# Performance work log

Hardware: AMD Instinct MI355X
Metric: run time of the kernel (lower is better)

## Reference

```python
import jax, jax.numpy as jnp
import numpy as np

N, E, D, K = 50000, 800000, 128, 128


def _graph_conv(x, src, dst, w, W_rel, b_rel, W_root, n_nodes):
    # PyG GraphConv (aggr='add'): out = lin_rel(sum_j w_ij * x_j) + lin_root(x)
    msg = w[:, None] * x[src]                              # [E, D]
    agg = jax.ops.segment_sum(msg, dst, num_segments=n_nodes)  # [N, D]
    return agg @ W_rel + b_rel + x @ W_root


def setup_inputs() -> dict:
    key = jax.random.key(0)
    ks = jax.random.split(key, 16)
    sc = 1.0 / np.sqrt(D).astype(np.float32)
    inp = {
        "x": jax.random.normal(ks[0], (N, D), dtype=jnp.float32),
        "edge_index": jax.random.randint(ks[1], (2, E), 0, N, dtype=jnp.int64 if jax.config.jax_enable_x64 else jnp.int32),
        "edge_weight": jax.random.uniform(ks[2], (E,), dtype=jnp.float32),
        # GraphConv layer 1
        "W_rel1": jax.random.normal(ks[3], (D, D), dtype=jnp.float32) * sc,
        "b_rel1": jnp.zeros((D,), dtype=jnp.float32),
        "W_root1": jax.random.normal(ks[4], (D, D), dtype=jnp.float32) * sc,
        # GraphConv layer 2
        "W_rel2": jax.random.normal(ks[5], (D, D), dtype=jnp.float32) * sc,
        "b_rel2": jnp.zeros((D,), dtype=jnp.float32),
        "W_root2": jax.random.normal(ks[6], (D, D), dtype=jnp.float32) * sc,
        # MLP: Linear(D,128) + Identity, then final Linear(128,K)
        "W_m1": jax.random.normal(ks[7], (D, 128), dtype=jnp.float32) * sc,
        "b_m1": jnp.zeros((128,), dtype=jnp.float32),
        "W_out": jax.random.normal(ks[8], (128, K), dtype=jnp.float32) * (1.0 / np.sqrt(128).astype(np.float32)),
        "b_out": jnp.zeros((K,), dtype=jnp.float32),
    }
    return inp


def reference(x, edge_index, edge_weight, W_rel1, b_rel1, W_root1,
              W_rel2, b_rel2, W_root2, W_m1, b_m1, W_out, b_out):
    n_nodes = x.shape[0]
    src, dst = edge_index[0], edge_index[1]

    # Message passing stack with ReLU
    h = jax.nn.relu(_graph_conv(x, src, dst, edge_weight, W_rel1, b_rel1, W_root1, n_nodes))
    h = jax.nn.relu(_graph_conv(h, src, dst, edge_weight, W_rel2, b_rel2, W_root2, n_nodes))

    # MLP -> cluster logits (mlp_act = Identity)
    s = (h @ W_m1 + b_m1) @ W_out + b_out                  # [N, K]
    probs = jax.nn.softmax(s, axis=-1)                     # [N, K]

    # dense_mincut_pool losses (computed edge-wise; A = to_dense_adj(edge_index, w))
    # degree d_i = sum_j A[i, j] = scatter of w over src
    deg = jax.ops.segment_sum(edge_weight, src, num_segments=n_nodes)  # [N]
    # mincut_num = trace(S^T A S) = sum_e w_e * <S[src_e], S[dst_e]>
    mincut_num = jnp.einsum('e,ek,ek->', edge_weight, probs[src], probs[dst])
    # mincut_den = trace(S^T D S) = sum_i d_i * ||S_i||^2
    mincut_den = jnp.sum(deg * jnp.sum(probs * probs, axis=-1))
    mc_loss = -(mincut_num / mincut_den)

    # orthogonality loss: || SS/||SS||_F - I/sqrt(K) ||_F
    ss = probs.T @ probs                                   # [K, K]
    k = probs.shape[1]
    o_loss = jnp.linalg.norm(ss / jnp.linalg.norm(ss) - jnp.eye(k, dtype=ss.dtype) / np.float32(np.sqrt(k)))

    return probs, mc_loss, o_loss
```

## Files before the change

### kernel.cpp

```cpp
#include <hip/hip_runtime.h>
#include <hip/hip_bf16.h>

#define D 128
#define KT 32
#define SS_BLOCKS 256
#define NUM_BLOCKS 2048

__device__ __forceinline__ float bfl(unsigned u) { return __uint_as_float(u << 16); }
__device__ __forceinline__ float bfh(unsigned u) { return __uint_as_float(u & 0xffff0000u); }
__device__ __forceinline__ unsigned short f2b(float f) {
    unsigned u = __float_as_uint(f);
    return (unsigned short)((u + 0x7fffu + ((u >> 16) & 1u)) >> 16);
}

__global__ __launch_bounds__(256) void f2bf_kernel(const float* __restrict__ in,
                                                   unsigned short* __restrict__ out, int n8) {
    int i = blockIdx.x * 256 + threadIdx.x;
    if (i < n8) {
        float4 a = ((const float4*)in)[2 * i];
        float4 b = ((const float4*)in)[2 * i + 1];
        ushort4 lo = make_ushort4(f2b(a.x), f2b(a.y), f2b(a.z), f2b(a.w));
        ushort4 hi = make_ushort4(f2b(b.x), f2b(b.y), f2b(b.z), f2b(b.w));
        ((ushort4*)out)[2 * i] = lo;
        ((ushort4*)out)[2 * i + 1] = hi;
    }
}

__global__ __launch_bounds__(256) void hist_deg_kernel(const int* __restrict__ src,
                                                       const int* __restrict__ dst,
                                                       const float* __restrict__ w,
                                                       int* __restrict__ cnt,
                                                       float* __restrict__ deg,
                                                       int* __restrict__ slot, int E) {
    int e = blockIdx.x * 256 + threadIdx.x;
    if (e < E) {
        slot[e] = atomicAdd(&cnt[dst[e]], 1);
        atomicAdd(&deg[src[e]], w[e]);
    }
}

__global__ __launch_bounds__(256) void scan_chunk_kernel(const int* __restrict__ cnt,
                                                         int* __restrict__ rowptr,
                                                         int* __restrict__ aux, int N) {
    __shared__ int ts[256];
    int t = threadIdx.x;
    int base = blockIdx.x * 1024 + t * 4;
    int v[4], s = 0;
#pragma unroll
    for (int i = 0; i < 4; ++i) {
        v[i] = (base + i < N) ? cnt[base + i] : 0;
        s += v[i];
    }
    ts[t] = s;
    __syncthreads();
#pragma unroll
    for (int off = 1; off < 256; off <<= 1) {
        int add = (t >= off) ? ts[t - off] : 0;
        __syncthreads();
        ts[t] += add;
        __syncthreads();
    }
    int run = ts[t] - s;
#pragma unroll
    for (int i = 0; i < 4; ++i) {
        run += v[i];
        if (base + i < N) rowptr[base + i + 1] = run;
    }
    if (t == 255) aux[blockIdx.x] = ts[255];
}

__global__ void scan_aux_kernel(int* __restrict__ aux, int nb) {
    if (threadIdx.x == 0) {
        int s = 0;
        for (int i = 0; i < nb; ++i) { s += aux[i]; aux[i] = s; }
    }
}

__global__ __launch_bounds__(256) void add_off_kernel(int* __restrict__ rowptr,
                                                      const int* __restrict__ aux, int N) {
    int i = blockIdx.x * 256 + threadIdx.x;
    if (i == 0) rowptr[0] = 0;
    if (i < N) {
        int b = i >> 10;
        if (b > 0) rowptr[i + 1] += aux[b - 1];
    }
}

__global__ __launch_bounds__(256) void fill_kernel(const int* __restrict__ src,
                                                   const int* __restrict__ dst,
                                                   const float* __restrict__ w,
                                                   const int* __restrict__ rowptr,
                                                   const int* __restrict__ slot,
                                                   int* __restrict__ csr_src,
                                                   float* __restrict__ csr_w, int E) {
    int e = blockIdx.x * 256 + threadIdx.x;
    if (e < E) {
        int pos = rowptr[dst[e]] + slot[e];
        csr_src[pos] = src[e];
        csr_w[pos] = w[e];
    }
}

__global__ __launch_bounds__(256) void gatherq_kernel(const unsigned short* __restrict__ xh,
                                                      const int* __restrict__ csr_src,
                                                      const float* __restrict__ csr_w,
                                                      const int* __restrict__ rowptr,
                                                      float* __restrict__ agg, int N) {
    int node = blockIdx.x * 4 + (threadIdx.x >> 6);
    if (node >= N) return;
    int lane = threadIdx.x & 63;
    int q = lane >> 4;
    int c8 = (lane & 15) * 8;
    int beg = rowptr[node], end = rowptr[node + 1];
    float a[4][8];
#pragma unroll
    for (int i = 0; i < 4; ++i)
#pragma unroll
        for (int k = 0; k < 8; ++k) a[i][k] = 0.f;
    int j = beg;
    for (; j + 15 < end; j += 16) {
        int si[4]; float wi[4]; uint4 qv[4];
#pragma unroll
        for (int i = 0; i < 4; ++i) {
            int e = j + 4 * i + q;
            si[i] = csr_src[e];
            wi[i] = csr_w[e];
        }
#pragma unroll
        for (int i = 0; i < 4; ++i) qv[i] = *(const uint4*)&xh[(size_t)si[i] * D + c8];
#pragma unroll
        for (int i = 0; i < 4; ++i) {
            a[i][0] += wi[i] * bfl(qv[i].x); a[i][1] += wi[i] * bfh(qv[i].x);
            a[i][2] += wi[i] * bfl(qv[i].y); a[i][3] += wi[i] * bfh(qv[i].y);
            a[i][4] += wi[i] * bfl(qv[i].z); a[i][5] += wi[i] * bfh(qv[i].z);
            a[i][6] += wi[i] * bfl(qv[i].w); a[i][7] += wi[i] * bfh(qv[i].w);
        }
    }
    for (; j + 3 < end; j += 4) {
        int e = j + q;
        int s0 = csr_src[e]; float w0 = csr_w[e];
        uint4 qv = *(const uint4*)&xh[(size_t)s0 * D + c8];
        a[0][0] += w0 * bfl(qv.x); a[0][1] += w0 * bfh(qv.x);
        a[0][2] += w0 * bfl(qv.y); a[0][3] += w0 * bfh(qv.y);
        a[0][4] += w0 * bfl(qv.z); a[0][5] += w0 * bfh(qv.z);
        a[0][6] += w0 * bfl(qv.w); a[0][7] += w0 * bfh(qv.w);
    }
    int rem = end - j;
    if (q < rem) {
        int e = j + q;
        int s0 = csr_src[e]; float w0 = csr_w[e];
        uint4 qv = *(const uint4*)&xh[(size_t)s0 * D + c8];
        a[1][0] += w0 * bfl(qv.x); a[1][1] += w0 * bfh(qv.x);
        a[1][2] += w0 * bfl(qv.y); a[1][3] += w0 * bfh(qv.y);
        a[1][4] += w0 * bfl(qv.z); a[1][5] += w0 * bfh(qv.z);
        a[1][6] += w0 * bfl(qv.w); a[1][7] += w0 * bfh(qv.w);
    }
    float r[8];
#pragma unroll
    for (int k = 0; k < 8; ++k) {
        r[k] = a[0][k] + a[1][k] + a[2][k] + a[3][k];
        r[k] += __shfl_xor(r[k], 16);
        r[k] += __shfl_xor(r[k], 32);
    }
    if (lane < 16) {
        *(float4*)&agg[(size_t)node * D + c8]     = make_float4(r[0], r[1], r[2], r[3]);
        *(float4*)&agg[(size_t)node * D + c8 + 4] = make_float4(r[4], r[5], r[6], r[7]);
    }
}

#define FMA4(acc, a, wv) { acc.x += (a) * (wv).x; acc.y += (a) * (wv).y; \
                           acc.z += (a) * (wv).z; acc.w += (a) * (wv).w; }

__global__ __launch_bounds__(256) void lin_kernel(const float* __restrict__ A1,
                                                  const float* __restrict__ A2,
                                                  const float* __restrict__ W1,
                                                  const float* __restrict__ W2,
                                                  const float* __restrict__ b,
                                                  float* __restrict__ out,
                                                  unsigned short* __restrict__ outh, int N) {
    __shared__ float As[KT][132];
    __shared__ float Ws[KT][D];
    int tid = threadIdx.x;
    int r0 = blockIdx.x * 128;
    int ty4 = (tid >> 3) * 4;
    int tx16 = (tid & 7) * 16;

    float4 acc[4][4];
#pragma unroll
    for (int i = 0; i < 4; ++i)
#pragma unroll
        for (int j = 0; j < 4; ++j) acc[i][j] = make_float4(0.f, 0.f, 0.f, 0.f);

    for (int t = 0; t < 8; ++t) {
        const float* A = (t < 4) ? A1 : A2;
        const float* W = (t < 4) ? W1 : W2;
        int koff = (t & 3) * KT;
        __syncthreads();
#pragma unroll
        for (int i = 0; i < 4; ++i) {
            int f4 = tid + i * 256;
            int row = f4 >> 3;
            int c4 = f4 & 7;
            float4 v = make_float4(0.f, 0.f, 0.f, 0.f);
            if (r0 + row < N) v = *(const float4*)&A[(size_t)(r0 + row) * D + koff + c4 * 4];
            As[c4 * 4 + 0][row] = v.x;
            As[c4 * 4 + 1][row] = v.y;
            As[c4 * 4 + 2][row] = v.z;
            As[c4 * 4 + 3][row] = v.w;
        }
#pragma unroll
        for (int i = 0; i < 4; ++i) {
            int f4 = tid + i * 256;
            int k = f4 >> 5;
            int c4 = f4 & 31;
            *(float4*)&Ws[k][c4 * 4] = *(const float4*)&W[(size_t)(koff + k) * D + c4 * 4];
        }
        __syncthreads();
#pragma unroll 4
        for (int k = 0; k < KT; ++k) {
            float4 av = *(const float4*)&As[k][ty4];
            float4 w0 = *(const float4*)&Ws[k][tx16];
            float4 w1 = *(const float4*)&Ws[k][tx16 + 4];
            float4 w2 = *(const float4*)&Ws[k][tx16 + 8];
            float4 w3 = *(const float4*)&Ws[k][tx16 + 12];
            FMA4(acc[0][0], av.x, w0); FMA4(acc[0][1], av.x, w1);
            FMA4(acc[0][2], av.x, w2); FMA4(acc[0][3], av.x, w3);
            FMA4(acc[1][0], av.y, w0); FMA4(acc[1][1], av.y, w1);
            FMA4(acc[1][2], av.y, w2); FMA4(acc[1][3], av.y, w3);
            FMA4(acc[2][0], av.z, w0); FMA4(acc[2][1], av.z, w1);
            FMA4(acc[2][2], av.z, w2); FMA4(acc[2][3], av.z, w3);
            FMA4(acc[3][0], av.w, w0); FMA4(acc[3][1], av.w, w1);
            FMA4(acc[3][2], av.w, w2); FMA4(acc[3][3], av.w, w3);
        }
    }
    float4 bv[4];
#pragma unroll
    for (int j = 0; j < 4; ++j) bv[j] = *(const float4*)&b[tx16 + j * 4];
#pragma unroll
    for (int i = 0; i < 4; ++i) {
        int r = r0 + ty4 + i;
        if (r < N) {
#pragma unroll
            for (int j = 0; j < 4; ++j) {
                float4 v;
                v.x = fmaxf(acc[i][j].x + bv[j].x, 0.f);
                v.y = fmaxf(acc[i][j].y + bv[j].y, 0.f);
                v.z = fmaxf(acc[i][j].z + bv[j].z, 0.f);
                v.w = fmaxf(acc[i][j].w + bv[j].w, 0.f);
                *(float4*)&out[(size_t)r * D + tx16 + j * 4] = v;
                if (outh) {
                    ushort4 u = make_ushort4(f2b(v.x), f2b(v.y), f2b(v.z), f2b(v.w));
                    *(ushort4*)&outh[(size_t)r * D + tx16 + j * 4] = u;
                }
            }
        }
    }
}

__global__ __launch_bounds__(256) void smallmm_kernel(const float* __restrict__ Wm1,
                                                      const float* __restrict__ bm1,
                                                      const float* __restrict__ Wout,
                                                      const float* __restrict__ bout,
                                                      float* __restrict__ Wc,
                                                      float* __restrict__ bc) {
    int idx = blockIdx.x * 256 + threadIdx.x;
    if (blockIdx.x < 64) {
        int i = idx >> 7, j = idx & 127;
        float s = 0.f;
        for (int k = 0; k < 128; ++k) s += Wm1[i * 128 + k] * Wout[k * 128 + j];
        Wc[idx] = s;
    } else {
        int j = threadIdx.x;
        if (j < 128) {
            float s = bout[j];
            for (int k = 0; k < 128; ++k) s += bm1[k] * Wout[k * 128 + j];
            bc[j] = s;
        }
    }
}

__global__ __launch_bounds__(256) void out_softmax_kernel(const float* __restrict__ h2,
                                                          const float* __restrict__ Wc,
                                                          const float* __restrict__ bc,
                                                          const float* __restrict__ deg,
                                                          float* __restrict__ probs,
                                                          unsigned short* __restrict__ pbh,
                                                          float* __restrict__ accum, int N) {
    __shared__ float Rs[32][128];
    __shared__ float Ws[128 * 64];
    int tid = threadIdx.x;
    int wave = tid >> 6, lane = tid & 63;
    int r0 = blockIdx.x * 32;
#pragma unroll
    for (int i = 0; i < 4; ++i) {
        int f4 = tid + i * 256;
        int row = f4 >> 5;
        int c4 = f4 & 31;
        float4 v = make_float4(0.f, 0.f, 0.f, 0.f);
        if (r0 + row < N) v = *(const float4*)&h2[(size_t)(r0 + row) * D + c4 * 4];
        *(float4*)&Rs[row][c4 * 4] = v;
    }
    float lg[8][2];
#pragma unroll
    for (int h = 0; h < 2; ++h) {
        __syncthreads();
#pragma unroll
        for (int i = 0; i < 8; ++i) {
            int f4 = tid + i * 256;
            int k = f4 >> 4;
            int c4 = f4 & 15;
            *(float4*)&Ws[k * 64 + c4 * 4] = *(const float4*)&Wc[(size_t)k * 128 + h * 64 + c4 * 4];
        }
        __syncthreads();
        float bv = bc[h * 64 + lane];
        float a[8];
#pragma unroll
        for (int ri = 0; ri < 8; ++ri) a[ri] = bv;
        for (int k = 0; k < 128; ++k) {
            float wv = Ws[k * 64 + lane];
#pragma unroll
            for (int ri = 0; ri < 8; ++ri) a[ri] += Rs[wave + ri * 4][k] * wv;
        }
#pragma unroll
        for (int ri = 0; ri < 8; ++ri) lg[ri][h] = a[ri];
    }
    float den_local = 0.f;
#pragma unroll
    for (int ri = 0; ri < 8; ++ri) {
        int row = wave + ri * 4;
        int gr = r0 + row;
        float m = fmaxf(lg[ri][0], lg[ri][1]);
#pragma unroll
        for (int s = 32; s >= 1; s >>= 1) m = fmaxf(m, __shfl_xor(m, s));
        float e0 = expf(lg[ri][0] - m);
        float e1 = expf(lg[ri][1] - m);
        float sum = e0 + e1;
#pragma unroll
        for (int s = 32; s >= 1; s >>= 1) sum += __shfl_xor(sum, s);
        float inv = 1.f / sum;
        float p0 = e0 * inv, p1 = e1 * inv;
        float sq = p0 * p0 + p1 * p1;
#pragma unroll
        for (int s = 32; s >= 1; s >>= 1) sq += __shfl_xor(sq, s);
        if (gr < N) {
            probs[(size_t)gr * D + lane]      = p0;
            probs[(size_t)gr * D + 64 + lane] = p1;
            pbh[(size_t)gr * D + lane]      = f2b(p0);
            pbh[(size_t)gr * D + 64 + lane] = f2b(p1);
            if (lane == 0) den_local += deg[gr] * sq;
        }
    }
    if (lane == 0 && den_local != 0.f) atomicAdd(&accum[1], den_local);
}

__global__ __launch_bounds__(256) void num_ss_kernel(const float* __restrict__ probs,
                                                     const unsigned short* __restrict__ pbh,
                                                     const int* __restrict__ csr_src,
                                                     const float* __restrict__ csr_w,
                                                     const int* __restrict__ rowptr,
                                                     float* __restrict__ accum,
                                                     float* __restrict__ partial, int N) {
    int tid = threadIdx.x;
    if (blockIdx.x < SS_BLOCKS) {
        __shared__ float Ps[32][132];
        int a0 = (tid >> 4) * 8;
        int b0 = (tid & 15) * 8;
        float acc[8][8];
#pragma unroll
        for (int i = 0; i < 8; ++i)
#pragma unroll
            for (int j = 0; j < 8; ++j) acc[i][j] = 0.f;

        int rowsPerBlk = (N + SS_BLOCKS - 1) / SS_BLOCKS;
        int rbeg = blockIdx.x * rowsPerBlk;
        int rend = rbeg + rowsPerBlk;
        if (rend > N) rend = N;

        for (int c = rbeg; c < rend; c += 32) {
            int nr = rend - c;
            if (nr > 32) nr = 32;
            __syncthreads();
            for (int i = tid; i < nr * 32; i += 256) {
                int r = i >> 5, c4 = i & 31;
                *(float4*)&Ps[r][c4 * 4] = *(const float4*)&probs[(size_t)(c + r) * D + c4 * 4];
            }
            __syncthreads();
            for (int r = 0; r < nr; ++r) {
                float4 av0 = *(const float4*)&Ps[r][a0];
                float4 av1 = *(const float4*)&Ps[r][a0 + 4];
                float4 bv0 = *(const float4*)&Ps[r][b0];
                float4 bv1 = *(const float4*)&Ps[r][b0 + 4];
                float av[8] = {av0.x, av0.y, av0.z, av0.w, av1.x, av1.y, av1.z, av1.w};
                float bv[8] = {bv0.x, bv0.y, bv0.z, bv0.w, bv1.x, bv1.y, bv1.z, bv1.w};
#pragma unroll
                for (int i = 0; i < 8; ++i)
#pragma unroll
                    for (int j = 0; j < 8; ++j) acc[i][j] += av[i] * bv[j];
            }
        }
        float* pb = partial + (size_t)blockIdx.x * 16384;
#pragma unroll
        for (int i = 0; i < 8; ++i) {
            *(float4*)&pb[(a0 + i) * 128 + b0]     = make_float4(acc[i][0], acc[i][1], acc[i][2], acc[i][3]);
            *(float4*)&pb[(a0 + i) * 128 + b0 + 4] = make_float4(acc[i][4], acc[i][5], acc[i][6], acc[i][7]);
        }
        return;
    }
    int bid = blockIdx.x - SS_BLOCKS;
    int wave = tid >> 6, lane = tid & 63;
    int q = lane >> 4;
    int c8 = (lane & 15) * 8;
    float acc = 0.f;
    int stride = NUM_BLOCKS * 4;
    for (int node = bid * 4 + wave; node < N; node += stride) {
        float4 pdA = *(const float4*)&probs[(size_t)node * D + c8];
        float4 pdB = *(const float4*)&probs[(size_t)node * D + c8 + 4];
        int beg = rowptr[node], end = rowptr[node + 1];
        int j = beg;
        for (; j + 15 < end; j += 16) {
            int si[4]; float wi[4]; uint4 qv[4];
#pragma unroll
            for (int i = 0; i < 4; ++i) {
                int e = j + 4 * i + q;
                si[i] = csr_src[e];
                wi[i] = csr_w[e];
            }
#pragma unroll
            for (int i = 0; i < 4; ++i) qv[i] = *(const uint4*)&pbh[(size_t)si[i] * D + c8];
#pragma unroll
            for (int i = 0; i < 4; ++i) {
                acc += wi[i] * (bfl(qv[i].x) * pdA.x + bfh(qv[i].x) * pdA.y
                              + bfl(qv[i].y) * pdA.z + bfh(qv[i].y) * pdA.w
                              + bfl(qv[i].z) * pdB.x + bfh(qv[i].z) * pdB.y
                              + bfl(qv[i].w) * pdB.z + bfh(qv[i].w) * pdB.w);
            }
        }
        for (; j + 3 < end; j += 4) {
            int e = j + q;
            int s0 = csr_src[e]; float w0 = csr_w[e];
            uint4 qv = *(const uint4*)&pbh[(size_t)s0 * D + c8];
            acc += w0 * (bfl(qv.x) * pdA.x + bfh(qv.x) * pdA.y
                       + bfl(qv.y) * pdA.z + bfh(qv.y) * pdA.w
                       + bfl(qv.z) * pdB.x + bfh(qv.z) * pdB.y
                       + bfl(qv.w) * pdB.z + bfh(qv.w) * pdB.w);
        }
        int rem = end - j;
        if (q < rem) {
            int e = j + q;
            int s0 = csr_src[e]; float w0 = csr_w[e];
            uint4 qv = *(const uint4*)&pbh[(size_t)s0 * D + c8];
            acc += w0 * (bfl(qv.x) * pdA.x + bfh(qv.x) * pdA.y
                       + bfl(qv.y) * pdA.z + bfh(qv.y) * pdA.w
                       + bfl(qv.z) * pdB.x + bfh(qv.z) * pdB.y
                       + bfl(qv.w) * pdB.z + bfh(qv.w) * pdB.w);
        }
    }
#pragma unroll
    for (int m = 32; m >= 1; m >>= 1) acc += __shfl_xor(acc, m);
    if (lane == 0 && acc != 0.f) atomicAdd(&accum[0], acc);
}

__global__ __launch_bounds__(256) void ss_reduce_kernel(const float* __restrict__ partial,
                                                        float* __restrict__ ss) {
    int i = blockIdx.x * 256 + threadIdx.x;
    float s = 0.f;
    for (int b = 0; b < SS_BLOCKS; ++b) s += partial[(size_t)b * 16384 + i];
    ss[i] = s;
}

__global__ __launch_bounds__(256) void finalize_kernel(const float* __restrict__ ss,
                                                       const float* __restrict__ accum,
                                                       float* __restrict__ out2) {
    int tid = threadIdx.x;
    __shared__ float wsum[4], wsum2[4];
    float s = 0.f;
    for (int i = tid; i < 16384; i += 256) { float v = ss[i]; s += v * v; }
#pragma unroll
    for (int m = 32; m >= 1; m >>= 1) s += __shfl_xor(s, m);
    if ((tid & 63) == 0) wsum[tid >> 6] = s;
    __syncthreads();
    float norm = sqrtf(wsum[0] + wsum[1] + wsum[2] + wsum[3]);
    float inv = 1.f / norm;
    const float rk = 0.08838834764831845f;
    float o = 0.f;
    for (int i = tid; i < 16384; i += 256) {
        int a = i >> 7, b = i & 127;
        float v = ss[i] * inv - (a == b ? rk : 0.f);
        o += v * v;
    }
#pragma unroll
    for (int m = 32; m >= 1; m >>= 1) o += __shfl_xor(o, m);
    if ((tid & 63) == 0) wsum2[tid >> 6] = o;
    __syncthreads();
    if (tid == 0) {
        out2[0] = -(accum[0] / accum[1]);
        out2[1] = sqrtf(wsum2[0] + wsum2[1] + wsum2[2] + wsum2[3]);
    }
}

extern "C" void kernel_launch(void* const* d_in, const int* in_sizes, int n_in,
                              void* d_out, int out_size, void* d_ws, size_t ws_size,
                              hipStream_t stream) {
    const float* x      = (const float*)d_in[0];
    const int*   ei     = (const int*)d_in[1];
    const float* w      = (const float*)d_in[2];
    const float* Wrel1  = (const float*)d_in[3];
    const float* brel1  = (const float*)d_in[4];
    const float* Wroot1 = (const float*)d_in[5];
    const float* Wrel2  = (const float*)d_in[6];
    const float* brel2  = (const float*)d_in[7];
    const float* Wroot2 = (const float*)d_in[8];
    const float* Wm1    = (const float*)d_in[9];
    const float* bm1    = (const float*)d_in[10];
    const float* Wout   = (const float*)d_in[11];
    const float* bout   = (const float*)d_in[12];

    int N = in_sizes[0] / D;
    int E = in_sizes[2];
    const int* src = ei;
    const int* dst = ei + E;

    float* probs = (float*)d_out;
    float* out2  = probs + (size_t)N * D;
    float* h2    = probs;

    float* ws    = (float*)d_ws;
    float* agg   = ws;
    float* h1    = ws + (size_t)N * D;
    float* Wc    = ws + (size_t)2 * N * D;
    float* bc    = Wc + 16384;
    float* ssb   = bc + 128;
    float* deg   = ssb + 16384;
    float* accum = deg + N;
    float* csr_w = accum + 2;
    int*   cnt   = (int*)(csr_w + E);
    int*   rowptr= cnt + N;
    int*   aux   = rowptr + N + 1;
    int*   csr_src = aux + 64;
    int*   slot  = csr_src + E;
    unsigned short* pbh = (unsigned short*)(slot + E);
    unsigned short* xh  = (unsigned short*)h1;

    hipMemsetAsync(deg, 0, (size_t)(N + 2) * sizeof(float), stream);
    hipMemsetAsync(cnt, 0, (size_t)N * sizeof(int), stream);

    int eGrid = (E + 255) / 256;
    int nb = (N + 1023) / 1024;
    int n8 = N * D / 8;

    f2bf_kernel<<<(n8 + 255) / 256, 256, 0, stream>>>(x, xh, n8);

    hist_deg_kernel<<<eGrid, 256, 0, stream>>>(src, dst, w, cnt, deg, slot, E);
    scan_chunk_kernel<<<nb, 256, 0, stream>>>(cnt, rowptr, aux, N);
    scan_aux_kernel<<<1, 64, 0, stream>>>(aux, nb);
    add_off_kernel<<<(N + 255) / 256, 256, 0, stream>>>(rowptr, aux, N);
    fill_kernel<<<eGrid, 256, 0, stream>>>(src, dst, w, rowptr, slot, csr_src, csr_w, E);

    gatherq_kernel<<<(N + 3) / 4, 256, 0, stream>>>(xh, csr_src, csr_w, rowptr, agg, N);
    lin_kernel<<<(N + 127) / 128, 256, 0, stream>>>(agg, x, Wrel1, Wroot1, brel1,
                                                    h1, pbh, N);
    gatherq_kernel<<<(N + 3) / 4, 256, 0, stream>>>(pbh, csr_src, csr_w, rowptr, agg, N);
    lin_kernel<<<(N + 127) / 128, 256, 0, stream>>>(agg, h1, Wrel2, Wroot2, brel2,
                                                    h2, (unsigned short*)nullptr, N);
    smallmm_kernel<<<65, 256, 0, stream>>>(Wm1, bm1, Wout, bout, Wc, bc);
    out_softmax_kernel<<<(N + 31) / 32, 256, 0, stream>>>(h2, Wc, bc, deg, probs, pbh, accum, N);
    num_ss_kernel<<<SS_BLOCKS + NUM_BLOCKS, 256, 0, stream>>>(probs, pbh, csr_src, csr_w,
                                                              rowptr, accum, agg, N);
    ss_reduce_kernel<<<64, 256, 0, stream>>>(agg, ssb);
    finalize_kernel<<<1, 256, 0, stream>>>(ssb, accum, out2);
}
```

Baseline: 620.2 us.

## Pack CSR src/weight into int2, fuse prep kernels, deepen gather unroll

Merges the fp32-to-bf16 conversion and the histogram/degree kernels into one launch by splitting the block index range. CSR source indices and edge weights are stored interleaved as int2, so each edge needs one 8-byte load instead of two separate loads. The gather and mincut-numerator loops now unroll over 32 edges (8 in flight per lane) instead of 16 to expose more memory-level parallelism. The wider unroll raises register pressure, and the 32-edge loop only runs for nodes of degree at least 32, which is rare with about 16 edges per node.

```diff
diff --git a/kernel.cpp b/kernel.cpp
--- a/kernel.cpp
+++ b/kernel.cpp
@@ -13,29 +13,32 @@
     return (unsigned short)((u + 0x7fffu + ((u >> 16) & 1u)) >> 16);
 }
 
-__global__ __launch_bounds__(256) void f2bf_kernel(const float* __restrict__ in,
-                                                   unsigned short* __restrict__ out, int n8) {
-    int i = blockIdx.x * 256 + threadIdx.x;
-    if (i < n8) {
-        float4 a = ((const float4*)in)[2 * i];
-        float4 b = ((const float4*)in)[2 * i + 1];
-        ushort4 lo = make_ushort4(f2b(a.x), f2b(a.y), f2b(a.z), f2b(a.w));
-        ushort4 hi = make_ushort4(f2b(b.x), f2b(b.y), f2b(b.z), f2b(b.w));
-        ((ushort4*)out)[2 * i] = lo;
-        ((ushort4*)out)[2 * i + 1] = hi;
-    }
-}
-
-__global__ __launch_bounds__(256) void hist_deg_kernel(const int* __restrict__ src,
-                                                       const int* __restrict__ dst,
-                                                       const float* __restrict__ w,
-                                                       int* __restrict__ cnt,
-                                                       float* __restrict__ deg,
-                                                       int* __restrict__ slot, int E) {
-    int e = blockIdx.x * 256 + threadIdx.x;
-    if (e < E) {
-        slot[e] = atomicAdd(&cnt[dst[e]], 1);
-        atomicAdd(&deg[src[e]], w[e]);
+__global__ __launch_bounds__(256) void pre_kernel(const float* __restrict__ x,
+                                                  unsigned short* __restrict__ xh,
+                                                  const int* __restrict__ src,
+                                                  const int* __restrict__ dst,
+                                                  const float* __restrict__ w,
+                                                  int* __restrict__ cnt,
+                                                  float* __restrict__ deg,
+                                                  int* __restrict__ slot,
+                                                  int E, int n8, int fGrid) {
+    int b = blockIdx.x;
+    if (b < fGrid) {
+        int i = b * 256 + threadIdx.x;
+        if (i < n8) {
+            float4 a = ((const float4*)x)[2 * i];
+            float4 c = ((const float4*)x)[2 * i + 1];
+            ushort4 lo = make_ushort4(f2b(a.x), f2b(a.y), f2b(a.z), f2b(a.w));
+            ushort4 hi = make_ushort4(f2b(c.x), f2b(c.y), f2b(c.z), f2b(c.w));
+            ((ushort4*)xh)[2 * i] = lo;
+            ((ushort4*)xh)[2 * i + 1] = hi;
+        }
+    } else {
+        int e = (b - fGrid) * 256 + threadIdx.x;
+        if (e < E) {
+            slot[e] = atomicAdd(&cnt[dst[e]], 1);
+            atomicAdd(&deg[src[e]], w[e]);
+        }
     }
 }
 
@@ -91,19 +94,16 @@
                                                    const float* __restrict__ w,
                                                    const int* __restrict__ rowptr,
                                                    const int* __restrict__ slot,
-                                                   int* __restrict__ csr_src,
-                                                   float* __restrict__ csr_w, int E) {
+                                                   int2* __restrict__ epk, int E) {
     int e = blockIdx.x * 256 + threadIdx.x;
     if (e < E) {
         int pos = rowptr[dst[e]] + slot[e];
-        csr_src[pos] = src[e];
-        csr_w[pos] = w[e];
+        epk[pos] = make_int2(src[e], __float_as_int(w[e]));
     }
 }
 
 __global__ __launch_bounds__(256) void gatherq_kernel(const unsigned short* __restrict__ xh,
-                                                      const int* __restrict__ csr_src,
-                                                      const float* __restrict__ csr_w,
+                                                      const int2* __restrict__ epk,
                                                       const int* __restrict__ rowptr,
                                                       float* __restrict__ agg, int N) {
     int node = blockIdx.x * 4 + (threadIdx.x >> 6);
@@ -118,28 +118,25 @@
 #pragma unroll
         for (int k = 0; k < 8; ++k) a[i][k] = 0.f;
     int j = beg;
-    for (; j + 15 < end; j += 16) {
-        int si[4]; float wi[4]; uint4 qv[4];
-#pragma unroll
-        for (int i = 0; i < 4; ++i) {
-            int e = j + 4 * i + q;
-            si[i] = csr_src[e];
-            wi[i] = csr_w[e];
-        }
-#pragma unroll
-        for (int i = 0; i < 4; ++i) qv[i] = *(const uint4*)&xh[(size_t)si[i] * D + c8];
-#pragma unroll
-        for (int i = 0; i < 4; ++i) {
-            a[i][0] += wi[i] * bfl(qv[i].x); a[i][1] += wi[i] * bfh(qv[i].x);
-            a[i][2] += wi[i] * bfl(qv[i].y); a[i][3] += wi[i] * bfh(qv[i].y);
-            a[i][4] += wi[i] * bfl(qv[i].z); a[i][5] += wi[i] * bfh(qv[i].z);
-            a[i][6] += wi[i] * bfl(qv[i].w); a[i][7] += wi[i] * bfh(qv[i].w);
+    for (; j + 31 < end; j += 32) {
+        int2 ed[8]; uint4 qv[8];
+#pragma unroll
+        for (int i = 0; i < 8; ++i) ed[i] = epk[j + 4 * i + q];
+#pragma unroll
+        for (int i = 0; i < 8; ++i) qv[i] = *(const uint4*)&xh[(size_t)ed[i].x * D + c8];
+#pragma unroll
+        for (int i = 0; i < 8; ++i) {
+            float w0 = __int_as_float(ed[i].y);
+            a[i & 3][0] += w0 * bfl(qv[i].x); a[i & 3][1] += w0 * bfh(qv[i].x);
+            a[i & 3][2] += w0 * bfl(qv[i].y); a[i & 3][3] += w0 * bfh(qv[i].y);
+            a[i & 3][4] += w0 * bfl(qv[i].z); a[i & 3][5] += w0 * bfh(qv[i].z);
+            a[i & 3][6] += w0 * bfl(qv[i].w); a[i & 3][7] += w0 * bfh(qv[i].w);
         }
     }
     for (; j + 3 < end; j += 4) {
-        int e = j + q;
-        int s0 = csr_src[e]; float w0 = csr_w[e];
-        uint4 qv = *(const uint4*)&xh[(size_t)s0 * D + c8];
+        int2 ed = epk[j + q];
+        float w0 = __int_as_float(ed.y);
+        uint4 qv = *(const uint4*)&xh[(size_t)ed.x * D + c8];
         a[0][0] += w0 * bfl(qv.x); a[0][1] += w0 * bfh(qv.x);
         a[0][2] += w0 * bfl(qv.y); a[0][3] += w0 * bfh(qv.y);
         a[0][4] += w0 * bfl(qv.z); a[0][5] += w0 * bfh(qv.z);
@@ -147,9 +144,9 @@
     }
     int rem = end - j;
     if (q < rem) {
-        int e = j + q;
-        int s0 = csr_src[e]; float w0 = csr_w[e];
-        uint4 qv = *(const uint4*)&xh[(size_t)s0 * D + c8];
+        int2 ed = epk[j + q];
+        float w0 = __int_as_float(ed.y);
+        uint4 qv = *(const uint4*)&xh[(size_t)ed.x * D + c8];
         a[1][0] += w0 * bfl(qv.x); a[1][1] += w0 * bfh(qv.x);
         a[1][2] += w0 * bfl(qv.y); a[1][3] += w0 * bfh(qv.y);
         a[1][4] += w0 * bfl(qv.z); a[1][5] += w0 * bfh(qv.z);
@@ -355,8 +352,7 @@
 
 __global__ __launch_bounds__(256) void num_ss_kernel(const float* __restrict__ probs,
                                                      const unsigned short* __restrict__ pbh,
-                                                     const int* __restrict__ csr_src,
-                                                     const float* __restrict__ csr_w,
+                                                     const int2* __restrict__ epk,
                                                      const int* __restrict__ rowptr,
                                                      float* __restrict__ accum,
                                                      float* __restrict__ partial, int N) {
@@ -417,28 +413,25 @@
         float4 pdB = *(const float4*)&probs[(size_t)node * D + c8 + 4];
         int beg = rowptr[node], end = rowptr[node + 1];
         int j = beg;
-        for (; j + 15 < end; j += 16) {
-            int si[4]; float wi[4]; uint4 qv[4];
-#pragma unroll
-            for (int i = 0; i < 4; ++i) {
-                int e = j + 4 * i + q;
-                si[i] = csr_src[e];
-                wi[i] = csr_w[e];
+        for (; j + 31 < end; j += 32) {
+            int2 ed[8]; uint4 qv[8];
+#pragma unroll
+            for (int i = 0; i < 8; ++i) ed[i] = epk[j + 4 * i + q];
+#pragma unroll
+            for (int i = 0; i < 8; ++i) qv[i] = *(const uint4*)&pbh[(size_t)ed[i].x * D + c8];
+#pragma unroll
+            for (int i = 0; i < 8; ++i) {
+                float w0 = __int_as_float(ed[i].y);
+                acc += w0 * (bfl(qv[i].x) * pdA.x + bfh(qv[i].x) * pdA.y
+                           + bfl(qv[i].y) * pdA.z + bfh(qv[i].y) * pdA.w
+                           + bfl(qv[i].z) * pdB.x + bfh(qv[i].z) * pdB.y
+                           + bfl(qv[i].w) * pdB.z + bfh(qv[i].w) * pdB.w);
             }
-#pragma unroll
-            for (int i = 0; i < 4; ++i) qv[i] = *(const uint4*)&pbh[(size_t)si[i] * D + c8];
-#pragma unroll
-            for (int i = 0; i < 4; ++i) {
-                acc += wi[i] * (bfl(qv[i].x) * pdA.x + bfh(qv[i].x) * pdA.y
-                              + bfl(qv[i].y) * pdA.z + bfh(qv[i].y) * pdA.w
-                              + bfl(qv[i].z) * pdB.x + bfh(qv[i].z) * pdB.y
-                              + bfl(qv[i].w) * pdB.z + bfh(qv[i].w) * pdB.w);
-            }
         }
         for (; j + 3 < end; j += 4) {
-            int e = j + q;
-            int s0 = csr_src[e]; float w0 = csr_w[e];
-            uint4 qv = *(const uint4*)&pbh[(size_t)s0 * D + c8];
+            int2 ed = epk[j + q];
+            float w0 = __int_as_float(ed.y);
+            uint4 qv = *(const uint4*)&pbh[(size_t)ed.x * D + c8];
             acc += w0 * (bfl(qv.x) * pdA.x + bfh(qv.x) * pdA.y
                        + bfl(qv.y) * pdA.z + bfh(qv.y) * pdA.w
                        + bfl(qv.z) * pdB.x + bfh(qv.z) * pdB.y
@@ -446,9 +439,9 @@
         }
         int rem = end - j;
         if (q < rem) {
-            int e = j + q;
-            int s0 = csr_src[e]; float w0 = csr_w[e];
-            uint4 qv = *(const uint4*)&pbh[(size_t)s0 * D + c8];
+            int2 ed = epk[j + q];
+            float w0 = __int_as_float(ed.y);
+            uint4 qv = *(const uint4*)&pbh[(size_t)ed.x * D + c8];
             acc += w0 * (bfl(qv.x) * pdA.x + bfh(qv.x) * pdA.y
                        + bfl(qv.y) * pdA.z + bfh(qv.y) * pdA.w
                        + bfl(qv.z) * pdB.x + bfh(qv.z) * pdB.y
@@ -532,12 +525,11 @@
     float* ssb   = bc + 128;
     float* deg   = ssb + 16384;
     float* accum = deg + N;
-    float* csr_w = accum + 2;
-    int*   cnt   = (int*)(csr_w + E);
+    int2*  epk   = (int2*)(accum + 2);
+    int*   cnt   = (int*)(epk + E);
     int*   rowptr= cnt + N;
     int*   aux   = rowptr + N + 1;
-    int*   csr_src = aux + 64;
-    int*   slot  = csr_src + E;
+    int*   slot  = aux + 64;
     unsigned short* pbh = (unsigned short*)(slot + E);
     unsigned short* xh  = (unsigned short*)h1;
 
@@ -547,24 +539,24 @@
     int eGrid = (E + 255) / 256;
     int nb = (N + 1023) / 1024;
     int n8 = N * D / 8;
-
-    f2bf_kernel<<<(n8 + 255) / 256, 256, 0, stream>>>(x, xh, n8);
-
-    hist_deg_kernel<<<eGrid, 256, 0, stream>>>(src, dst, w, cnt, deg, slot, E);
+    int fGrid = (n8 + 255) / 256;
+
+    pre_kernel<<<fGrid + eGrid, 256, 0, stream>>>(x, xh, src, dst, w, cnt, deg, slot,
+                                                  E, n8, fGrid);
     scan_chunk_kernel<<<nb, 256, 0, stream>>>(cnt, rowptr, aux, N);
     scan_aux_kernel<<<1, 64, 0, stream>>>(aux, nb);
     add_off_kernel<<<(N + 255) / 256, 256, 0, stream>>>(rowptr, aux, N);
-    fill_kernel<<<eGrid, 256, 0, stream>>>(src, dst, w, rowptr, slot, csr_src, csr_w, E);
-
-    gatherq_kernel<<<(N + 3) / 4, 256, 0, stream>>>(xh, csr_src, csr_w, rowptr, agg, N);
+    fill_kernel<<<eGrid, 256, 0, stream>>>(src, dst, w, rowptr, slot, epk, E);
+
+    gatherq_kernel<<<(N + 3) / 4, 256, 0, stream>>>(xh, epk, rowptr, agg, N);
     lin_kernel<<<(N + 127) / 128, 256, 0, stream>>>(agg, x, Wrel1, Wroot1, brel1,
                                                     h1, pbh, N);
-    gatherq_kernel<<<(N + 3) / 4, 256, 0, stream>>>(pbh, csr_src, csr_w, rowptr, agg, N);
+    gatherq_kernel<<<(N + 3) / 4, 256, 0, stream>>>(pbh, epk, rowptr, agg, N);
     lin_kernel<<<(N + 127) / 128, 256, 0, stream>>>(agg, h1, Wrel2, Wroot2, brel2,
                                                     h2, (unsigned short*)nullptr, N);
     smallmm_kernel<<<65, 256, 0, stream>>>(Wm1, bm1, Wout, bout, Wc, bc);
     out_softmax_kernel<<<(N + 31) / 32, 256, 0, stream>>>(h2, Wc, bc, deg, probs, pbh, accum, N);
-    num_ss_kernel<<<SS_BLOCKS + NUM_BLOCKS, 256, 0, stream>>>(probs, pbh, csr_src, csr_w,
+    num_ss_kernel<<<SS_BLOCKS + NUM_BLOCKS, 256, 0, stream>>>(probs, pbh, epk,
                                                               rowptr, accum, agg, N);
     ss_reduce_kernel<<<64, 256, 0, stream>>>(agg, ssb);
     finalize_kernel<<<1, 256, 0, stream>>>(ssb, accum, out2);
```

After: 657.2 us. 1.06x slower.
